# Performance work log

Measured on AMD Instinct MI355X. Metric: run time of the kernel, lower is better.

## Reference

```python
import jax, jax.numpy as jnp
import numpy as np

B, TC, TQ, D = 32, 2048, 256, 256

def setup_inputs() -> dict:
    key = jax.random.key(0)
    k1, k2, k3 = jax.random.split(key, 3)
    context_emb = jax.random.normal(k1, (B, TC, D), dtype=jnp.float32)
    query_emb = jax.random.normal(k2, (B, TQ, D), dtype=jnp.float32)
    # nn.Linear(3d, 1, bias=False) weight flattened to [3d]
    w = jax.random.normal(k3, (3 * D,), dtype=jnp.float32) * (1.0 / np.sqrt(3 * D))
    return {"context_emb": context_emb, "query_emb": query_emb, "w": w}

def reference(context_emb, query_emb, w):
    d = context_emb.shape[-1]
    w1, w2, w3 = w[:d], w[d:2*d], w[2*d:]
    # Trilinear similarity S[b,t,q] = c.w1 + q.w2 + (c*q).w3 -- equivalent to
    # Linear over cat(c_ext, q_ext, c_ext*q_ext) without materializing [B,Tc,Tq,3d].
    S = (jnp.einsum('btd,d->bt', context_emb, w1)[:, :, None]
         + jnp.einsum('bqd,d->bq', query_emb, w2)[:, None, :]
         + jnp.einsum('btd,bqd->btq', context_emb * w3, query_emb))  # [B,Tc,Tq]
    S_softmax_row = jax.nn.softmax(S, axis=2)              # [B,Tc,Tq]
    b_t = jax.nn.softmax(jnp.max(S, axis=2), axis=1)       # [B,Tc]
    U_attention = jnp.einsum('btq,bqd->btd', S_softmax_row, query_emb)  # [B,Tc,d]
    h = jnp.einsum('bt,btd->bd', b_t, context_emb)         # [B,d]
    H_attention = h[:, None, :]                            # broadcast over Tc
    G = jnp.concatenate(
        (context_emb,
         U_attention,
         context_emb * U_attention,
         context_emb * H_attention), axis=-1)              # [B,Tc,4d]
    return G
```

## Files before the change

kernel.cpp:

```cpp
#include <hip/hip_runtime.h>

#define NB  32
#define NTC 2048
#define NTQ 256
#define ND  256

#define HP2_OFF 0
#define H_OFF   266240
#define Q2_OFF  274432
#define QBF_OFF 282624
#define QT_OFF  (282624 + 1048576)

#define PSTR 264
#define USTR 130

typedef __attribute__((ext_vector_type(8))) short short8v;
typedef __attribute__((ext_vector_type(4))) float float4v;
typedef unsigned int u32;

static __device__ inline short f2bf(float f) {
  union { float f; unsigned u; } v; v.f = f;
  unsigned r = v.u + 0x7FFFu + ((v.u >> 16) & 1u);
  return (short)(r >> 16);
}

static __device__ inline void gload_lds16(const short* g, short* l) {
  __builtin_amdgcn_global_load_lds(
      (const __attribute__((address_space(1))) u32*)g,
      (__attribute__((address_space(3))) u32*)l, 16, 0, 0);
}

__global__ __launch_bounds__(256) void k0_prep(const float* __restrict__ qry,
                                               const float* __restrict__ w,
                                               float* __restrict__ q2_ws,
                                               short* __restrict__ Qbf,
                                               short* __restrict__ Qt) {
  __shared__ float sRed[8][32];
  const int tid = threadIdx.x;
  const int b = blockIdx.x >> 3;
  const int q0 = (blockIdx.x & 7) << 5;
  const int q = tid & 31;
  const int dc = tid >> 5;
  const float* src = qry + (((size_t)b * NTQ) + q0 + q) * ND + dc * 32;
  const float* w2p = w + ND + dc * 32;

  float vals[32];
  float part = 0.f;
  #pragma unroll
  for (int i = 0; i < 8; ++i) {
    float4 v = *(const float4*)(src + 4 * i);
    float4 u = *(const float4*)(w2p + 4 * i);
    part += v.x*u.x + v.y*u.y + v.z*u.z + v.w*u.w;
    vals[4*i] = v.x; vals[4*i+1] = v.y; vals[4*i+2] = v.z; vals[4*i+3] = v.w;
  }
  short pk[32];
  #pragma unroll
  for (int i = 0; i < 32; ++i) pk[i] = f2bf(vals[i]);

  short* dst = Qbf + ((size_t)b * NTQ + q0 + q) * ND + dc * 32;
  #pragma unroll
  for (int i = 0; i < 4; ++i) *(short8v*)(dst + 8 * i) = *(short8v*)(pk + 8 * i);
  short* dstT = Qt + (size_t)b * NTQ * ND + q0 + q;
  #pragma unroll
  for (int i = 0; i < 32; ++i) dstT[(size_t)(dc * 32 + i) * NTQ] = pk[i];

  part += __shfl_xor(part, 32);
  if ((tid & 32) == 0) sRed[dc][q] = part;
  __syncthreads();
  if (tid < 32) {
    float s = sRed[0][tid] + sRed[2][tid] + sRed[4][tid] + sRed[6][tid];
    q2_ws[b * NTQ + q0 + tid] = s;
  }
}

__global__ __launch_bounds__(256, 2) void k1_main(const float* __restrict__ ctx,
                                                  const float* __restrict__ w,
                                                  const short* __restrict__ Qbf,
                                                  const short* __restrict__ Qt,
                                                  const float* __restrict__ q2_ws,
                                                  float* __restrict__ hp2,
                                                  float* __restrict__ G) {
  __shared__ __align__(16) short sStage[2][256 * 32];
  __shared__ __align__(16) short sP_all[4 * 16 * PSTR];
  __shared__ __align__(16) float sW[768];

  const int tid  = threadIdx.x;
  const int wv   = tid >> 6;
  const int lane = tid & 63;
  const int g    = lane >> 4;
  const int li   = lane & 15;
  const int bid  = blockIdx.x;
  const int obid = (bid & 7) * 128 + (bid >> 3);
  const int b    = obid >> 5;
  const int tile = obid & 31;
  const int t0   = tile << 6;

  short* sPw = sP_all + wv * (16 * PSTR);
  float* sUw = (float*)sPw;
  float* sH    = (float*)sStage;
  float* sMm   = (float*)sStage + 1024;
  float* sRedM = (float*)sStage + 1088;
  float* sRedZ = (float*)sStage + 1092;

  const float* __restrict__ ctxB = ctx + ((size_t)b * NTC + t0) * ND;
  const short* __restrict__ Qb   = Qbf + (size_t)b * NTQ * ND;
  const short* __restrict__ Qtb  = Qt  + (size_t)b * NTQ * ND;

  const int srow = 64 * wv + (lane >> 2);
  const int sblk = lane & 3;

  #define STAGE(buf, src, c0)                                                   \
    { _Pragma("unroll")                                                         \
      for (int j = 0; j < 4; ++j) {                                             \
        const int row_ = srow + 16 * j;                                         \
        const int gi_  = sblk ^ ((row_ >> 1) & 3);                              \
        gload_lds16((src) + (size_t)row_ * 256 + (c0) + 8 * gi_,                \
                    &sStage[buf][wv * 2048 + j * 512]);                         \
      } }

  float4v acc[16];
  #pragma unroll
  for (int n = 0; n < 16; ++n) acc[n] = (float4v)0.f;
  float s1part = 0.f;

  float q2v[16];
  #pragma unroll
  for (int n = 0; n < 16; ++n) q2v[n] = q2_ws[b * NTQ + 16 * n + li];
  if (tid < 192) *(float4*)(sW + 4 * tid) = *(const float4*)(w + 4 * tid);
  STAGE(0, Qb, 0);
  const float* arow = ctxB + (size_t)(16 * wv + li) * ND + 8 * g;
  float4 Ac0 = *(const float4*)(arow);
  float4 Ac1 = *(const float4*)(arow + 4);
  asm volatile("s_waitcnt vmcnt(0) lgkmcnt(0)" ::: "memory");
  __builtin_amdgcn_s_barrier();
  __builtin_amdgcn_sched_barrier(0);

  const size_t gb0 = ((size_t)b * NTC + t0 + 16 * wv + li) * 1024 + 8 * g;

  #pragma unroll
  for (int c = 0; c < 8; ++c) {
    float4 u0 = *(const float4*)(sW + 32 * c + 8 * g);
    float4 u1 = *(const float4*)(sW + 32 * c + 8 * g + 4);
    float4 v0 = *(const float4*)(sW + 512 + 32 * c + 8 * g);
    float4 v1 = *(const float4*)(sW + 512 + 32 * c + 8 * g + 4);
    s1part += Ac0.x*u0.x + Ac0.y*u0.y + Ac0.z*u0.z + Ac0.w*u0.w
            + Ac1.x*u1.x + Ac1.y*u1.y + Ac1.z*u1.z + Ac1.w*u1.w;
    short8v af;
    af[0]=f2bf(Ac0.x*v0.x); af[1]=f2bf(Ac0.y*v0.y); af[2]=f2bf(Ac0.z*v0.z); af[3]=f2bf(Ac0.w*v0.w);
    af[4]=f2bf(Ac1.x*v1.x); af[5]=f2bf(Ac1.y*v1.y); af[6]=f2bf(Ac1.z*v1.z); af[7]=f2bf(Ac1.w*v1.w);
    __builtin_amdgcn_sched_barrier(0);
    float4 An0, An1;
    if (c < 7) {
      An0 = *(const float4*)(arow + 32 * (c + 1));
      An1 = *(const float4*)(arow + 32 * (c + 1) + 4);
    }
    __builtin_amdgcn_sched_barrier(0);
    if (c < 7) { STAGE((c + 1) & 1, Qb, 32 * (c + 1)); }
    else       { STAGE(0, Qtb, 0); }
    __builtin_amdgcn_sched_barrier(0);
    asm volatile("s_waitcnt vmcnt(6)" ::: "memory");
    __builtin_amdgcn_s_barrier();
    __builtin_amdgcn_sched_barrier(0);
    const short* sb = sStage[c & 1];
    #pragma unroll
    for (int n = 0; n < 16; ++n) {
      const int row = 16 * n + li;
      short8v bb = *(const short8v*)(sb + row * 32 + 8 * (g ^ ((row >> 1) & 3)));
      acc[n] = __builtin_amdgcn_mfma_f32_16x16x32_bf16(af, bb, acc[n], 0, 0, 0);
    }
    *(float4*)(G + gb0 + 32 * c)     = Ac0;
    *(float4*)(G + gb0 + 32 * c + 4) = Ac1;
    __builtin_amdgcn_sched_barrier(0);
    __builtin_amdgcn_s_barrier();
    __builtin_amdgcn_sched_barrier(0);
    Ac0 = An0; Ac1 = An1;
  }

  s1part += __shfl_xor(s1part, 16);
  s1part += __shfl_xor(s1part, 32);
  float s1r[4];
  #pragma unroll
  for (int r = 0; r < 4; ++r) s1r[r] = __shfl(s1part, 4 * g + r);

  #pragma unroll
  for (int n = 0; n < 16; ++n)
    #pragma unroll
    for (int r = 0; r < 4; ++r) acc[n][r] += s1r[r] + q2v[n];

  float mx[4], inv[4];
  #pragma unroll
  for (int r = 0; r < 4; ++r) {
    float m0 = acc[0][r];
    #pragma unroll
    for (int n = 1; n < 16; ++n) m0 = fmaxf(m0, acc[n][r]);
    m0 = fmaxf(m0, __shfl_xor(m0, 1));
    m0 = fmaxf(m0, __shfl_xor(m0, 2));
    m0 = fmaxf(m0, __shfl_xor(m0, 4));
    m0 = fmaxf(m0, __shfl_xor(m0, 8));
    mx[r] = m0;
  }
  #pragma unroll
  for (int r = 0; r < 4; ++r) {
    float z = 0.f;
    #pragma unroll
    for (int n = 0; n < 16; ++n) { float e = __expf(acc[n][r] - mx[r]); acc[n][r] = e; z += e; }
    z += __shfl_xor(z, 1);
    z += __shfl_xor(z, 2);
    z += __shfl_xor(z, 4);
    z += __shfl_xor(z, 8);
    inv[r] = 1.0f / z;
  }
  #pragma unroll
  for (int n = 0; n < 16; ++n) {
    #pragma unroll
    for (int r = 0; r < 4; ++r)
      sPw[(4 * g + r) * PSTR + 16 * n + li] = f2bf(acc[n][r] * inv[r]);
  }

  float4v acc2[16];
  #pragma unroll
  for (int n = 0; n < 16; ++n) acc2[n] = (float4v)0.f;

  #pragma unroll
  for (int cc = 0; cc < 8; ++cc) {
    short8v a2 = *(const short8v*)(sPw + li * PSTR + 32 * cc + 8 * g);
    __builtin_amdgcn_sched_barrier(0);
    if (cc < 7) { STAGE((cc + 1) & 1, Qtb, 32 * (cc + 1)); }
    __builtin_amdgcn_sched_barrier(0);
    if (cc < 7) asm volatile("s_waitcnt vmcnt(4)" ::: "memory");
    else        asm volatile("s_waitcnt vmcnt(0)" ::: "memory");
    __builtin_amdgcn_s_barrier();
    __builtin_amdgcn_sched_barrier(0);
    const short* sb = sStage[cc & 1];
    #pragma unroll
    for (int n = 0; n < 16; ++n) {
      const int row = 16 * n + li;
      short8v bb = *(const short8v*)(sb + row * 32 + 8 * (g ^ ((row >> 1) & 3)));
      acc2[n] = __builtin_amdgcn_mfma_f32_16x16x32_bf16(a2, bb, acc2[n], 0, 0, 0);
    }
    __builtin_amdgcn_sched_barrier(0);
    __builtin_amdgcn_s_barrier();
    __builtin_amdgcn_sched_barrier(0);
  }

  if (li == 0) {
    #pragma unroll
    for (int r = 0; r < 4; ++r) sMm[16 * wv + 4 * g + r] = mx[r];
  }
  float lm = fmaxf(fmaxf(mx[0], mx[1]), fmaxf(mx[2], mx[3]));
  lm = fmaxf(lm, __shfl_xor(lm, 16));
  lm = fmaxf(lm, __shfl_xor(lm, 32));
  if (lane == 0) sRedM[wv] = lm;
  __syncthreads();
  const float Mloc = fmaxf(fmaxf(sRedM[0], sRedM[1]), fmaxf(sRedM[2], sRedM[3]));
  float zp = 0.f;
  #pragma unroll
  for (int r = 0; r < 4; ++r) zp += __expf(mx[r] - Mloc);
  zp += __shfl_xor(zp, 16);
  zp += __shfl_xor(zp, 32);
  if (lane == 0) sRedZ[wv] = zp;
  float wgt[4];
  #pragma unroll
  for (int k = 0; k < 4; ++k) wgt[k] = __expf(sMm[16 * wv + 4 * k + g] - Mloc);

  float4 ha[2][2];
  #pragma unroll
  for (int h = 0; h < 2; ++h)
    #pragma unroll
    for (int j = 0; j < 2; ++j) ha[h][j] = make_float4(0.f, 0.f, 0.f, 0.f);

  asm volatile("s_waitcnt lgkmcnt(0)" ::: "memory");
  __builtin_amdgcn_sched_barrier(0);
  #pragma unroll
  for (int h = 0; h < 2; ++h) {
    #pragma unroll
    for (int nn = 0; nn < 8; ++nn) {
      const int n = 8 * h + nn;
      #pragma unroll
      for (int r = 0; r < 4; ++r)
        sUw[(4 * g + r) * USTR + 16 * nn + li] = acc2[n][r];
    }
    asm volatile("s_waitcnt lgkmcnt(0)" ::: "memory");
    __builtin_amdgcn_sched_barrier(0);
    #pragma unroll
    for (int r0 = 0; r0 < 16; r0 += 4) {
      const int row = r0 + g;
      const float wk = wgt[r0 >> 2];
      #pragma unroll
      for (int j = 0; j < 2; ++j) {
        float4 u = *(const float4*)(sUw + row * USTR + 64 * j + 4 * li);
        const int gcol = 128 * h + 64 * j + 4 * li;
        const float* cp = ctxB + (size_t)(16 * wv + row) * ND + gcol;
        float4 c = *(const float4*)cp;
        const size_t gb = ((size_t)b * NTC + t0 + 16 * wv + row) * 1024 + gcol;
        *(float4*)(G + gb + 256) = u;
        *(float4*)(G + gb + 512) = make_float4(c.x*u.x, c.y*u.y, c.z*u.z, c.w*u.w);
        ha[h][j].x += wk * c.x; ha[h][j].y += wk * c.y;
        ha[h][j].z += wk * c.z; ha[h][j].w += wk * c.w;
      }
    }
    asm volatile("s_waitcnt lgkmcnt(0)" ::: "memory");
    __builtin_amdgcn_sched_barrier(0);
  }

  #pragma unroll
  for (int h = 0; h < 2; ++h)
    #pragma unroll
    for (int j = 0; j < 2; ++j) {
      float* f = (float*)&ha[h][j];
      #pragma unroll
      for (int e = 0; e < 4; ++e) {
        f[e] += __shfl_xor(f[e], 16);
        f[e] += __shfl_xor(f[e], 32);
      }
    }
  if (g == 0) {
    #pragma unroll
    for (int h = 0; h < 2; ++h)
      #pragma unroll
      for (int j = 0; j < 2; ++j)
        *(float4*)(sH + wv * 256 + 128 * h + 64 * j + 4 * li) = ha[h][j];
  }
  __syncthreads();
  float* hp = hp2 + (size_t)(b * 32 + tile) * 260;
  {
    float ph = sH[tid & 255] + sH[256 + (tid & 255)] + sH[512 + (tid & 255)] + sH[768 + (tid & 255)];
    if (tid < 256) hp[tid] = ph;
  }
  if (tid == 0) {
    hp[256] = Mloc;
    hp[257] = sRedZ[0] + sRedZ[1] + sRedZ[2] + sRedZ[3];
  }
  #undef STAGE
}

__global__ __launch_bounds__(256) void k2h(const float* __restrict__ hp2,
                                           float* __restrict__ h_ws) {
  __shared__ float sM2[32], sZ2[32];
  const int b = blockIdx.x;
  const int tid = threadIdx.x;
  if (tid < 32) {
    sM2[tid] = hp2[(size_t)(b * 32 + tid) * 260 + 256];
    sZ2[tid] = hp2[(size_t)(b * 32 + tid) * 260 + 257];
  }
  __syncthreads();
  float M = -1e30f;
  #pragma unroll
  for (int i = 0; i < 32; ++i) M = fmaxf(M, sM2[i]);
  float Z = 0.f;
  float a = 0.f;
  #pragma unroll
  for (int i = 0; i < 32; ++i) {
    float e = __expf(sM2[i] - M);
    Z += sZ2[i] * e;
    a += hp2[(size_t)(b * 32 + i) * 260 + tid] * e;
  }
  h_ws[b * 256 + tid] = a / Z;
}

__global__ __launch_bounds__(256) void k3_epi(const float* __restrict__ ctx,
                                              const float* __restrict__ h_ws,
                                              float* __restrict__ G) {
  size_t f = (size_t)blockIdx.x * 256 + threadIdx.x;
  size_t e = f * 4;
  int d = (int)(e & 255);
  size_t bt = e >> 8;
  int b = (int)(bt >> 11);
  float4 c = *(const float4*)(ctx + e);
  float4 h = *(const float4*)(h_ws + b * ND + d);
  *(float4*)(G + bt * 1024 + 768 + d) =
      make_float4(c.x * h.x, c.y * h.y, c.z * h.z, c.w * h.w);
}

extern "C" void kernel_launch(void* const* d_in, const int* in_sizes, int n_in,
                              void* d_out, int out_size, void* d_ws, size_t ws_size,
                              hipStream_t stream) {
  const float* ctx = (const float*)d_in[0];
  const float* qry = (const float*)d_in[1];
  const float* w   = (const float*)d_in[2];
  float* G  = (float*)d_out;
  float* ws = (float*)d_ws;
  float* hp2   = ws + HP2_OFF;
  float* h_ws  = ws + H_OFF;
  float* q2_ws = ws + Q2_OFF;
  short* Qbf = (short*)(ws + QBF_OFF);
  short* Qt  = (short*)(ws + QT_OFF);

  k0_prep<<<NB * 8, 256, 0, stream>>>(qry, w, q2_ws, Qbf, Qt);
  k1_main<<<NB * (NTC / 64), 256, 0, stream>>>(ctx, w, Qbf, Qt, q2_ws, hp2, G);
  k2h<<<NB, 256, 0, stream>>>(hp2, h_ws);
  k3_epi<<<16384, 256, 0, stream>>>(ctx, h_ws, G);
}
```

Before: 108.2 us.

## Restructure P·Q GEMM to tile over output columns and drain U per chunk

The second GEMM (softmax P times Q) now stages Q-transpose in 32-output-column chunks with a new swizzle and loops over the full K dimension inside each chunk. Each 32-column slice of U is written straight to G together with c*U and the h partial sums. This replaces the 16-register-tile accumulator and the LDS transpose round-trip through sUw. The aim is lower register pressure and no extra LDS staging of U, at the cost of narrower, scalar G stores and more LDS B-fragment reads per chunk.

Measured after the change: 103.5 us. 4.4% less time.

```diff
diff --git a/kernel.cpp b/kernel.cpp
--- a/kernel.cpp
+++ b/kernel.cpp
@@ -12,7 +12,6 @@
 #define QT_OFF  (282624 + 1048576)
 
 #define PSTR 264
-#define USTR 130
 
 typedef __attribute__((ext_vector_type(8))) short short8v;
 typedef __attribute__((ext_vector_type(4))) float float4v;
@@ -83,6 +82,8 @@
   __shared__ __align__(16) short sStage[2][256 * 32];
   __shared__ __align__(16) short sP_all[4 * 16 * PSTR];
   __shared__ __align__(16) float sW[768];
+  __shared__ __align__(16) float sHall[4][256];
+  __shared__ float sRedM[4], sRedZ[4];
 
   const int tid  = threadIdx.x;
   const int wv   = tid >> 6;
@@ -96,11 +97,6 @@
   const int t0   = tile << 6;
 
   short* sPw = sP_all + wv * (16 * PSTR);
-  float* sUw = (float*)sPw;
-  float* sH    = (float*)sStage;
-  float* sMm   = (float*)sStage + 1024;
-  float* sRedM = (float*)sStage + 1088;
-  float* sRedZ = (float*)sStage + 1092;
 
   const float* __restrict__ ctxB = ctx + ((size_t)b * NTC + t0) * ND;
   const short* __restrict__ Qb   = Qbf + (size_t)b * NTQ * ND;
@@ -115,6 +111,16 @@
         const int row_ = srow + 16 * j;                                         \
         const int gi_  = sblk ^ ((row_ >> 1) & 3);                              \
         gload_lds16((src) + (size_t)row_ * 256 + (c0) + 8 * gi_,                \
+                    &sStage[buf][wv * 2048 + j * 512]);                         \
+      } }
+
+  #define STAGE2(buf, cc)                                                       \
+    { _Pragma("unroll")                                                         \
+      for (int j = 0; j < 4; ++j) {                                             \
+        const int slot_ = (wv * 4 + j) * 64 + lane;                             \
+        const int row_  = slot_ >> 5;                                           \
+        const int gr_   = slot_ & 31;                                           \
+        gload_lds16(Qtb + (size_t)(32 * (cc) + row_) * 256 + 8 * (gr_ ^ (row_ & 7)), \
                     &sStage[buf][wv * 2048 + j * 512]);                         \
       } }
 
@@ -156,7 +162,7 @@
     }
     __builtin_amdgcn_sched_barrier(0);
     if (c < 7) { STAGE((c + 1) & 1, Qb, 32 * (c + 1)); }
-    else       { STAGE(0, Qtb, 0); }
+    else       { STAGE2(0, 0); }
     __builtin_amdgcn_sched_barrier(0);
     asm volatile("s_waitcnt vmcnt(6)" ::: "memory");
     __builtin_amdgcn_s_barrier();
@@ -217,121 +223,82 @@
       sPw[(4 * g + r) * PSTR + 16 * n + li] = f2bf(acc[n][r] * inv[r]);
   }
 
-  float4v acc2[16];
-  #pragma unroll
-  for (int n = 0; n < 16; ++n) acc2[n] = (float4v)0.f;
-
-  #pragma unroll
-  for (int cc = 0; cc < 8; ++cc) {
-    short8v a2 = *(const short8v*)(sPw + li * PSTR + 32 * cc + 8 * g);
-    __builtin_amdgcn_sched_barrier(0);
-    if (cc < 7) { STAGE((cc + 1) & 1, Qtb, 32 * (cc + 1)); }
-    __builtin_amdgcn_sched_barrier(0);
-    if (cc < 7) asm volatile("s_waitcnt vmcnt(4)" ::: "memory");
-    else        asm volatile("s_waitcnt vmcnt(0)" ::: "memory");
-    __builtin_amdgcn_s_barrier();
-    __builtin_amdgcn_sched_barrier(0);
-    const short* sb = sStage[cc & 1];
-    #pragma unroll
-    for (int n = 0; n < 16; ++n) {
-      const int row = 16 * n + li;
-      short8v bb = *(const short8v*)(sb + row * 32 + 8 * (g ^ ((row >> 1) & 3)));
-      acc2[n] = __builtin_amdgcn_mfma_f32_16x16x32_bf16(a2, bb, acc2[n], 0, 0, 0);
-    }
-    __builtin_amdgcn_sched_barrier(0);
-    __builtin_amdgcn_s_barrier();
-    __builtin_amdgcn_sched_barrier(0);
-  }
-
-  if (li == 0) {
-    #pragma unroll
-    for (int r = 0; r < 4; ++r) sMm[16 * wv + 4 * g + r] = mx[r];
-  }
   float lm = fmaxf(fmaxf(mx[0], mx[1]), fmaxf(mx[2], mx[3]));
   lm = fmaxf(lm, __shfl_xor(lm, 16));
   lm = fmaxf(lm, __shfl_xor(lm, 32));
   if (lane == 0) sRedM[wv] = lm;
-  __syncthreads();
+  __builtin_amdgcn_sched_barrier(0);
+  asm volatile("s_waitcnt lgkmcnt(0)" ::: "memory");
+  __builtin_amdgcn_s_barrier();
+  __builtin_amdgcn_sched_barrier(0);
   const float Mloc = fmaxf(fmaxf(sRedM[0], sRedM[1]), fmaxf(sRedM[2], sRedM[3]));
+  float wgt[4];
   float zp = 0.f;
   #pragma unroll
-  for (int r = 0; r < 4; ++r) zp += __expf(mx[r] - Mloc);
+  for (int r = 0; r < 4; ++r) { wgt[r] = __expf(mx[r] - Mloc); zp += wgt[r]; }
   zp += __shfl_xor(zp, 16);
   zp += __shfl_xor(zp, 32);
   if (lane == 0) sRedZ[wv] = zp;
-  float wgt[4];
-  #pragma unroll
-  for (int k = 0; k < 4; ++k) wgt[k] = __expf(sMm[16 * wv + 4 * k + g] - Mloc);
-
-  float4 ha[2][2];
-  #pragma unroll
-  for (int h = 0; h < 2; ++h)
-    #pragma unroll
-    for (int j = 0; j < 2; ++j) ha[h][j] = make_float4(0.f, 0.f, 0.f, 0.f);
-
-  asm volatile("s_waitcnt lgkmcnt(0)" ::: "memory");
-  __builtin_amdgcn_sched_barrier(0);
-  #pragma unroll
-  for (int h = 0; h < 2; ++h) {
-    #pragma unroll
-    for (int nn = 0; nn < 8; ++nn) {
-      const int n = 8 * h + nn;
-      #pragma unroll
-      for (int r = 0; r < 4; ++r)
-        sUw[(4 * g + r) * USTR + 16 * nn + li] = acc2[n][r];
-    }
-    asm volatile("s_waitcnt lgkmcnt(0)" ::: "memory");
-    __builtin_amdgcn_sched_barrier(0);
-    #pragma unroll
-    for (int r0 = 0; r0 < 16; r0 += 4) {
-      const int row = r0 + g;
-      const float wk = wgt[r0 >> 2];
-      #pragma unroll
-      for (int j = 0; j < 2; ++j) {
-        float4 u = *(const float4*)(sUw + row * USTR + 64 * j + 4 * li);
-        const int gcol = 128 * h + 64 * j + 4 * li;
-        const float* cp = ctxB + (size_t)(16 * wv + row) * ND + gcol;
-        float4 c = *(const float4*)cp;
-        const size_t gb = ((size_t)b * NTC + t0 + 16 * wv + row) * 1024 + gcol;
-        *(float4*)(G + gb + 256) = u;
-        *(float4*)(G + gb + 512) = make_float4(c.x*u.x, c.y*u.y, c.z*u.z, c.w*u.w);
-        ha[h][j].x += wk * c.x; ha[h][j].y += wk * c.y;
-        ha[h][j].z += wk * c.z; ha[h][j].w += wk * c.w;
-      }
-    }
-    asm volatile("s_waitcnt lgkmcnt(0)" ::: "memory");
-    __builtin_amdgcn_sched_barrier(0);
-  }
-
-  #pragma unroll
-  for (int h = 0; h < 2; ++h)
-    #pragma unroll
-    for (int j = 0; j < 2; ++j) {
-      float* f = (float*)&ha[h][j];
-      #pragma unroll
-      for (int e = 0; e < 4; ++e) {
-        f[e] += __shfl_xor(f[e], 16);
-        f[e] += __shfl_xor(f[e], 32);
-      }
-    }
-  if (g == 0) {
-    #pragma unroll
-    for (int h = 0; h < 2; ++h)
-      #pragma unroll
-      for (int j = 0; j < 2; ++j)
-        *(float4*)(sH + wv * 256 + 128 * h + 64 * j + 4 * li) = ha[h][j];
-  }
+
+  #pragma unroll
+  for (int cc = 0; cc < 8; ++cc) {
+    if (cc < 7) { STAGE2((cc + 1) & 1, cc + 1); }
+    __builtin_amdgcn_sched_barrier(0);
+    if (cc < 7) asm volatile("s_waitcnt vmcnt(4)" ::: "memory");
+    else        asm volatile("s_waitcnt vmcnt(0)" ::: "memory");
+    __builtin_amdgcn_s_barrier();
+    __builtin_amdgcn_sched_barrier(0);
+    const short* sb = sStage[cc & 1];
+    float4v uacc0 = (float4v)0.f, uacc1 = (float4v)0.f;
+    #pragma unroll
+    for (int ks = 0; ks < 8; ++ks) {
+      short8v a2 = *(const short8v*)(sPw + li * PSTR + 32 * ks + 8 * g);
+      short8v b0 = *(const short8v*)(sb + (li)      * 256 + 8 * ((4 * ks + g) ^ (li & 7)));
+      short8v b1 = *(const short8v*)(sb + (16 + li) * 256 + 8 * ((4 * ks + g) ^ (li & 7)));
+      uacc0 = __builtin_amdgcn_mfma_f32_16x16x32_bf16(a2, b0, uacc0, 0, 0, 0);
+      uacc1 = __builtin_amdgcn_mfma_f32_16x16x32_bf16(a2, b1, uacc1, 0, 0, 0);
+    }
+    __builtin_amdgcn_sched_barrier(0);
+    __builtin_amdgcn_s_barrier();
+    __builtin_amdgcn_sched_barrier(0);
+    float hc0 = 0.f, hc1 = 0.f;
+    #pragma unroll
+    for (int r = 0; r < 4; ++r) {
+      const int trow = 16 * wv + 4 * g + r;
+      const size_t gb = ((size_t)b * NTC + t0 + trow) * 1024 + 32 * cc;
+      const float* cp = ctxB + (size_t)trow * ND + 32 * cc;
+      const float c0 = cp[li];
+      const float c1 = cp[16 + li];
+      const float uu0 = uacc0[r];
+      const float uu1 = uacc1[r];
+      G[gb + 256 + li]      = uu0;
+      G[gb + 256 + 16 + li] = uu1;
+      G[gb + 512 + li]      = c0 * uu0;
+      G[gb + 512 + 16 + li] = c1 * uu1;
+      hc0 += wgt[r] * c0;
+      hc1 += wgt[r] * c1;
+    }
+    hc0 += __shfl_xor(hc0, 16); hc0 += __shfl_xor(hc0, 32);
+    hc1 += __shfl_xor(hc1, 16); hc1 += __shfl_xor(hc1, 32);
+    if (g == 0) {
+      sHall[wv][32 * cc + li]      = hc0;
+      sHall[wv][32 * cc + 16 + li] = hc1;
+    }
+  }
+
   __syncthreads();
   float* hp = hp2 + (size_t)(b * 32 + tile) * 260;
   {
-    float ph = sH[tid & 255] + sH[256 + (tid & 255)] + sH[512 + (tid & 255)] + sH[768 + (tid & 255)];
-    if (tid < 256) hp[tid] = ph;
+    const int d = tid & 255;
+    float ph = sHall[0][d] + sHall[1][d] + sHall[2][d] + sHall[3][d];
+    hp[d] = ph;
   }
   if (tid == 0) {
     hp[256] = Mloc;
     hp[257] = sRedZ[0] + sRedZ[1] + sRedZ[2] + sRedZ[3];
   }
   #undef STAGE
+  #undef STAGE2
 }
 
 __global__ __launch_bounds__(256) void k2h(const float* __restrict__ hp2,
```
